# Performance work log

Measured on AMD Instinct MI355X. Metric: run time of the kernel, lower is better.

## Reference

```python
import jax, jax.numpy as jnp
import numpy as np

D_MODEL = 2048
NUM_HEADS = 16
D_K = D_MODEL // NUM_HEADS
LORA_R = 8
LORA_ALPHA = 16
SCALING = LORA_ALPHA / LORA_R  # 2.0
B, S = 2, 2048


def setup_inputs() -> dict:
    key = jax.random.key(0)
    ks = jax.random.split(key, 17)
    s = 1.0 / np.sqrt(D_MODEL)
    d = {"x": jax.random.normal(ks[0], (B, S, D_MODEL), jnp.float32)}
    i = 1
    for name in ("q", "k", "v", "o"):
        d[f"W{name}"] = jax.random.uniform(ks[i], (D_MODEL, D_MODEL), jnp.float32, -s, s); i += 1
        d[f"b{name}"] = jax.random.uniform(ks[i], (D_MODEL,), jnp.float32, -s, s); i += 1
        d[f"A{name}"] = jax.random.uniform(ks[i], (LORA_R, D_MODEL), jnp.float32, -s, s); i += 1
        # lora_B is zero-initialized in the module, but use small random so grads flow meaningfully
        d[f"B{name}"] = jax.random.normal(ks[i], (D_MODEL, LORA_R), jnp.float32) * 0.01; i += 1
    return d


def _lora_linear(x, W, b, A, Bm):
    # F.linear(x, W, b) + (x @ A.T @ B.T) * scaling
    return x @ W.T + b + ((x @ A.T) @ Bm.T) * SCALING


def reference(x, Wq, bq, Aq, Bq, Wk, bk, Ak, Bk, Wv, bv, Av, Bv, Wo, bo, Ao, Bo):
    batch = x.shape[0]
    q = _lora_linear(x, Wq, bq, Aq, Bq)
    k = _lora_linear(x, Wk, bk, Ak, Bk)
    v = _lora_linear(x, Wv, bv, Av, Bv)
    # [B, S, H, Dk] -> [B, H, S, Dk]
    q = q.reshape(batch, -1, NUM_HEADS, D_K).transpose(0, 2, 1, 3)
    k = k.reshape(batch, -1, NUM_HEADS, D_K).transpose(0, 2, 1, 3)
    v = v.reshape(batch, -1, NUM_HEADS, D_K).transpose(0, 2, 1, 3)
    scores = jnp.einsum("bhqd,bhkd->bhqk", q, k) / jnp.sqrt(jnp.float32(D_K))
    attn = jax.nn.softmax(scores, axis=-1)
    context = jnp.einsum("bhqk,bhkd->bhqd", attn, v)
    context = context.transpose(0, 2, 1, 3).reshape(batch, -1, D_MODEL)
    return _lora_linear(context, Wo, bo, Ao, Bo)
```

## Files before the change

### kernel.cpp

```cpp
#include <hip/hip_runtime.h>
#include <stdint.h>

typedef unsigned short u16;
typedef unsigned int   u32;
typedef __bf16  bf16x8 __attribute__((ext_vector_type(8)));
typedef float   f32x4  __attribute__((ext_vector_type(4)));

#define LORA_SCALE 2.0f
#define QSCALE 0.08838834764831845f
#define LOG2E  1.4426950408889634f
#define RESCALE_THR 8.0f

__device__ __forceinline__ u16 f2bf(float f){
  u32 u = __builtin_bit_cast(u32, f);
  u32 r = (u + 0x7fffu + ((u >> 16) & 1u)) >> 16;
  return (u16)r;
}
__device__ __forceinline__ float bf2f(u16 v){
  return __builtin_bit_cast(float, ((u32)v) << 16);
}
__device__ __forceinline__ u32 cvt_pk_bf16(float lo, float hi){
  u32 d;
  asm("v_cvt_pk_bf16_f32 %0, %1, %2" : "=v"(d) : "v"(lo), "v"(hi));
  return d;
}

typedef __attribute__((address_space(3))) u32 lds_u32_t;
typedef __attribute__((address_space(1))) const u32 g_u32_t;

__device__ __forceinline__ void gload16(const void* g, void* l){
  __builtin_amdgcn_global_load_lds((g_u32_t*)(unsigned long long)g,
                                   (lds_u32_t*)(u32)(unsigned long long)l,
                                   16, 0, 0);
}

__global__ __launch_bounds__(256) void cvt_w4(const float* __restrict__ W0,
    const float* __restrict__ W1, const float* __restrict__ W2,
    const float* __restrict__ W3, u16* __restrict__ wqkv, u16* __restrict__ wo){
  int sel = blockIdx.x >> 11;
  int inner = blockIdx.x & 2047;
  const float* src = sel==0 ? W0 : sel==1 ? W1 : sel==2 ? W2 : W3;
  u16* dst = sel<3 ? (wqkv + (size_t)sel*4194304) : wo;
  int i = (inner*256 + threadIdx.x) * 8;
  float4 a = *(const float4*)(src + i);
  float4 b = *(const float4*)(src + i + 4);
  u16 o[8] = {f2bf(a.x),f2bf(a.y),f2bf(a.z),f2bf(a.w),
              f2bf(b.x),f2bf(b.y),f2bf(b.z),f2bf(b.w)};
  *(uint4*)(dst + i) = *(const uint4*)o;
}

__global__ __launch_bounds__(256) void lora_x_fused(const float* __restrict__ x,
    const float* __restrict__ A0, const float* __restrict__ A1, const float* __restrict__ A2,
    float* __restrict__ xout, u16* __restrict__ xbf){
  int w = threadIdx.x >> 6, lane = threadIdx.x & 63;
  int m = blockIdx.x * 4 + w;
  float acc[3][8];
  #pragma unroll
  for (int g=0; g<3; ++g)
    #pragma unroll
    for (int r=0; r<8; ++r) acc[g][r] = 0.f;
  const float* As[3] = {A0, A1, A2};
  #pragma unroll 1
  for (int it=0; it<8; ++it){
    int k = it*256 + lane*4;
    float4 xv = *(const float4*)(x + (size_t)m*2048 + k);
    u16 o[4] = {f2bf(xv.x), f2bf(xv.y), f2bf(xv.z), f2bf(xv.w)};
    *(uint2*)(xbf + (size_t)m*2048 + k) = *(const uint2*)o;
    #pragma unroll
    for (int g=0; g<3; ++g){
      const float* Ag = As[g];
      #pragma unroll
      for (int r=0; r<8; ++r){
        float4 av = *(const float4*)(Ag + r*2048 + k);
        acc[g][r] += xv.x*av.x + xv.y*av.y + xv.z*av.z + xv.w*av.w;
      }
    }
  }
  #pragma unroll
  for (int g=0; g<3; ++g)
    #pragma unroll
    for (int r=0; r<8; ++r){
      float v = acc[g][r];
      #pragma unroll
      for (int off=32; off; off>>=1) v += __shfl_xor(v, off);
      if (lane == 0) xout[g*32768 + m*8 + r] = v;
    }
}

__global__ __launch_bounds__(256) void lora_xa_bf16(const u16* __restrict__ xin,
    const float* __restrict__ A0, float* __restrict__ xout){
  int w = threadIdx.x >> 6, lane = threadIdx.x & 63;
  int m = blockIdx.x * 4 + w;
  float acc[8];
  #pragma unroll
  for (int r=0; r<8; ++r) acc[r] = 0.f;
  #pragma unroll 1
  for (int it=0; it<8; ++it){
    int k = it*256 + lane*4;
    ushort4 u = *(const ushort4*)(xin + (size_t)m*2048 + k);
    float4 xv = {bf2f(u.x), bf2f(u.y), bf2f(u.z), bf2f(u.w)};
    #pragma unroll
    for (int r=0; r<8; ++r){
      float4 av = *(const float4*)(A0 + r*2048 + k);
      acc[r] += xv.x*av.x + xv.y*av.y + xv.z*av.z + xv.w*av.w;
    }
  }
  #pragma unroll
  for (int r=0; r<8; ++r){
    float v = acc[r];
    #pragma unroll
    for (int off=32; off; off>>=1) v += __shfl_xor(v, off);
    if (lane == 0) xout[m*8 + r] = v;
  }
}

__device__ __forceinline__ void gemm_core_v7(
    const u16* __restrict__ Aptr,
    const u16* __restrict__ Wptr,
    u16* lds, int tid, f32x4 acc[8][4]){
  const int Kd = 2048;
  int l = tid & 63, w = tid >> 6;
  int l15 = l & 15, l4 = l >> 4;
  int wm = w >> 1, wn = w & 1;
  char* L = (char*)lds;
  int wb = w * 1024;
  const u16* asrc[4]; const u16* bsrc[2];
  #pragma unroll
  for (int i=0;i<4;i++){ int row=(i*4+w)*16+(l>>2); int sc=((l&3)^((row>>1)&3))<<3;
    asrc[i] = Aptr + (size_t)row*Kd + sc; }
  #pragma unroll
  for (int i=0;i<2;i++){ int row=(i*4+w)*16+(l>>2); int sc=((l&3)^((row>>1)&3))<<3;
    bsrc[i] = Wptr + (size_t)row*Kd + sc; }
  int aoff[8], boff[4];
  #pragma unroll
  for (int mr=0;mr<8;mr++){ int ra=wm*128+mr*16+l15; aoff[mr]=ra*64+((l4^((ra>>1)&3))<<4); }
  #pragma unroll
  for (int nr=0;nr<4;nr++){ int rb=wn*64+nr*16+l15; boff[nr]=16384+rb*64+((l4^((rb>>1)&3))<<4); }

  auto STG = [&](int kt, int sbase){
    char* D = L + sbase;
    gload16(asrc[0]+kt, D +        wb);
    gload16(asrc[1]+kt, D +  4096+ wb);
    gload16(asrc[2]+kt, D +  8192+ wb);
    gload16(asrc[3]+kt, D + 12288+ wb);
    gload16(bsrc[0]+kt, D + 16384+ wb);
    gload16(bsrc[1]+kt, D + 20480+ wb);
  };

  STG(0, 0); STG(32, 24576);
  asm volatile("s_waitcnt vmcnt(6)" ::: "memory");
  __builtin_amdgcn_s_barrier();

  int bb = 0, sb = 49152, kt2 = 64;
  #pragma unroll 1
  for (int t = 0; t < 64; ++t){
    bf16x8 af[4], bf[4];
    #pragma unroll
    for (int mr=0;mr<4;mr++) af[mr] = *(const bf16x8*)(L + bb + aoff[mr]);
    #pragma unroll
    for (int nr=0;nr<4;nr++) bf[nr] = *(const bf16x8*)(L + bb + boff[nr]);
    if (t < 62) STG(kt2, sb);
    __builtin_amdgcn_s_barrier();
    __builtin_amdgcn_s_setprio(1);
    #pragma unroll
    for (int mr=0;mr<4;mr++)
      #pragma unroll
      for (int nr=0;nr<4;nr++)
        acc[mr][nr] = __builtin_amdgcn_mfma_f32_16x16x32_bf16(af[mr], bf[nr], acc[mr][nr], 0,0,0);
    __builtin_amdgcn_s_setprio(0);
    __builtin_amdgcn_s_barrier();
    bf16x8 ag[4];
    #pragma unroll
    for (int mr=0;mr<4;mr++) ag[mr] = *(const bf16x8*)(L + bb + aoff[mr+4]);
    if (t < 62)       asm volatile("s_waitcnt vmcnt(6)" ::: "memory");
    else if (t == 62) asm volatile("s_waitcnt vmcnt(0)" ::: "memory");
    __builtin_amdgcn_s_barrier();
    __builtin_amdgcn_s_setprio(1);
    #pragma unroll
    for (int mr=0;mr<4;mr++)
      #pragma unroll
      for (int nr=0;nr<4;nr++)
        acc[mr+4][nr] = __builtin_amdgcn_mfma_f32_16x16x32_bf16(ag[mr], bf[nr], acc[mr+4][nr], 0,0,0);
    __builtin_amdgcn_s_setprio(0);
    __builtin_amdgcn_s_barrier();
    bb = (bb == 49152) ? 0 : bb + 24576;
    sb = (sb == 49152) ? 0 : sb + 24576;
    kt2 += 32;
  }
}

__global__ __launch_bounds__(256, 2) void gemm_qkv(
    const u16* __restrict__ A, const u16* __restrict__ W,
    const float* __restrict__ bq, const float* __restrict__ bk, const float* __restrict__ bv,
    const float* __restrict__ lBq, const float* __restrict__ lBk, const float* __restrict__ lBv,
    const float* __restrict__ xa, u16* __restrict__ Qb, u16* __restrict__ Kb, u16* __restrict__ Vb){
  __shared__ u16 lds[36864];
  int tid = threadIdx.x;
  int l = tid & 63, w = tid >> 6;
  int l15 = l & 15, l4 = l >> 4;
  int wm = w >> 1, wn = w & 1;
  int bid = blockIdx.x;
  int virt = (bid & 7) * 96 + (bid >> 3);
  int mt = virt & 15, nt = virt >> 4;
  int m0 = mt * 256, n0g = nt * 128;
  int which = nt >> 4;
  int n0 = (nt & 15) * 128;
  const float* bias = which==0 ? bq : which==1 ? bk : bv;
  const float* lB   = which==0 ? lBq : which==1 ? lBk : lBv;
  const float* xs   = xa + which*32768;
  u16* outp         = which==0 ? Qb : which==1 ? Kb : Vb;
  int swz = (which <= 1);
  float oscale = (which == 0) ? QSCALE*LOG2E : 1.0f;

  f32x4 acc[8][4];
  #pragma unroll
  for (int mr=0; mr<8; mr++)
    #pragma unroll
    for (int nr=0; nr<4; nr++) acc[mr][nr] = (f32x4){0.f,0.f,0.f,0.f};

  gemm_core_v7(A + (size_t)m0*2048, W + (size_t)n0g*2048, lds, tid, acc);

  float bvv[4]; float4 lb0[4], lb1[4];
  #pragma unroll
  for (int nr=0; nr<4; nr++){
    int col = n0 + wn*64 + nr*16 + l15;
    bvv[nr] = bias[col];
    lb0[nr] = *(const float4*)(lB + col*8);
    lb1[nr] = *(const float4*)(lB + col*8 + 4);
  }
  #pragma unroll
  for (int mr=0; mr<8; mr++)
    #pragma unroll
    for (int j=0; j<4; j++){
      int r = m0 + wm*128 + mr*16 + l4*4 + j;
      float4 xv0 = *(const float4*)(xs + (size_t)r*8);
      float4 xv1 = *(const float4*)(xs + (size_t)r*8 + 4);
      #pragma unroll
      for (int nr=0; nr<4; nr++){
        int col = n0 + wn*64 + nr*16 + l15;
        float v = acc[mr][nr][j] + bvv[nr] + LORA_SCALE * (
            xv0.x*lb0[nr].x + xv0.y*lb0[nr].y + xv0.z*lb0[nr].z + xv0.w*lb0[nr].w +
            xv1.x*lb1[nr].x + xv1.y*lb1[nr].y + xv1.z*lb1[nr].z + xv1.w*lb1[nr].w);
        v *= oscale;
        int cs = swz ? (col ^ ((r & 7) << 3)) : col;
        outp[(size_t)r*2048 + cs] = f2bf(v);
      }
    }
}

__global__ __launch_bounds__(256, 2) void gemm_o(
    const u16* __restrict__ A, const u16* __restrict__ W,
    const float* __restrict__ bias, const float* __restrict__ lB,
    const float* __restrict__ xa, float* __restrict__ outp){
  __shared__ u16 lds[36864];
  int tid = threadIdx.x;
  int l = tid & 63, w = tid >> 6;
  int l15 = l & 15, l4 = l >> 4;
  int wm = w >> 1, wn = w & 1;
  int bid = blockIdx.x;
  int virt = (bid & 7) * 32 + (bid >> 3);
  int mt = virt & 15, nt = virt >> 4;
  int m0 = mt * 256, n0 = nt * 128;

  f32x4 acc[8][4];
  #pragma unroll
  for (int mr=0; mr<8; mr++)
    #pragma unroll
    for (int nr=0; nr<4; nr++) acc[mr][nr] = (f32x4){0.f,0.f,0.f,0.f};

  gemm_core_v7(A + (size_t)m0*2048, W + (size_t)n0*2048, lds, tid, acc);

  float bv[4]; float4 lb0[4], lb1[4];
  #pragma unroll
  for (int nr=0; nr<4; nr++){
    int col = n0 + wn*64 + nr*16 + l15;
    bv[nr] = bias[col];
    lb0[nr] = *(const float4*)(lB + col*8);
    lb1[nr] = *(const float4*)(lB + col*8 + 4);
  }
  #pragma unroll
  for (int mr=0; mr<8; mr++)
    #pragma unroll
    for (int j=0; j<4; j++){
      int r = m0 + wm*128 + mr*16 + l4*4 + j;
      float4 xv0 = *(const float4*)(xa + (size_t)r*8);
      float4 xv1 = *(const float4*)(xa + (size_t)r*8 + 4);
      #pragma unroll
      for (int nr=0; nr<4; nr++){
        int col = n0 + wn*64 + nr*16 + l15;
        float v = acc[mr][nr][j] + bv[nr] + LORA_SCALE * (
            xv0.x*lb0[nr].x + xv0.y*lb0[nr].y + xv0.z*lb0[nr].z + xv0.w*lb0[nr].w +
            xv1.x*lb1[nr].x + xv1.y*lb1[nr].y + xv1.z*lb1[nr].z + xv1.w*lb1[nr].w);
        outp[(size_t)r*2048 + col] = v;
      }
    }
}

__global__ __launch_bounds__(256) void transpose_v(const u16* __restrict__ V,
                                                   u16* __restrict__ Vt){
  __shared__ u16 tile[64*80];
  int tid = threadIdx.x;
  int f0 = blockIdx.x * 64, m0 = blockIdx.y * 64;
  int i = tid >> 2, j0 = (tid & 3) * 16;
  #pragma unroll
  for (int kk=0; kk<16; kk+=8){
    uint4 u = *(const uint4*)(V + (size_t)(m0 + i)*2048 + f0 + j0 + kk);
    *(uint4*)(tile + i*80 + j0 + kk) = u;
  }
  __syncthreads();
  int j = tid >> 2, i0 = (tid & 3) * 16;
  int b = m0 >> 11, s0 = m0 & 2047;
  int h = f0 >> 7, d = (f0 & 127) + j;
  int c = (d & 7) << 3;
  size_t obase = ((size_t)((b*16 + h)*128 + d)) * 2048 + s0;
  #pragma unroll
  for (int kk=0; kk<16; kk+=8){
    u16 v8[8];
    #pragma unroll
    for (int u2=0; u2<8; ++u2) v8[u2] = tile[(i0+kk+u2)*80 + j];
    *(uint4*)(Vt + obase + ((i0+kk) ^ c)) = *(const uint4*)v8;
  }
}

__global__ __launch_bounds__(256, 2) void attn_kernel(
    const u16* __restrict__ Q, const u16* __restrict__ K,
    const u16* __restrict__ Vt, u16* __restrict__ ctx){
  __shared__ u16 buf[2][16384];
  __shared__ u16 Psh[4*32*64];
  int tid = threadIdx.x, w = tid >> 6, lane = tid & 63;
  int l15 = lane & 15, l4 = lane >> 4;
  int lin = blockIdx.x;
  int virt = (lin & 7) * 64 + (lin >> 3);
  int qt = virt & 15, bh = virt >> 4;
  int b = bh >> 4, h = bh & 15;
  const u16* Qg = Q + (size_t)(b*2048 + qt*128) * 2048 + h*128;
  const u16* Kg = K + (size_t)(b*2048) * 2048 + h*128;
  const u16* Vg = Vt + (size_t)bh * 128 * 2048;

  #pragma unroll
  for (int i=0; i<8; ++i){
    int e = (i*256 + tid) * 8;
    int r = e >> 7, cc = e & 127;
    gload16(Qg + (size_t)r*2048 + cc, (char*)buf[1] + i*4096 + w*1024);
  }
  #pragma unroll
  for (int i=0; i<4; ++i){
    int e = (i*256 + tid) * 8;
    int r = e >> 7, cc = e & 127;
    gload16(Kg + (size_t)r*2048 + cc, (char*)buf[0] + i*4096 + w*1024);
    int dd = e >> 6, c2 = e & 63;
    gload16(Vg + (size_t)dd*2048 + c2, (char*)buf[0] + 16384 + i*4096 + w*1024);
  }
  __syncthreads();

  bf16x8 qf[2][4];
  #pragma unroll
  for (int mi=0; mi<2; mi++){
    int r = w*32 + mi*16 + l15;
    #pragma unroll
    for (int kb=0; kb<4; kb++){
      int cc = (kb*32 + l4*8) ^ ((r & 7) << 3);
      qf[mi][kb] = *(const bf16x8*)(buf[1] + r*128 + cc);
    }
  }
  __syncthreads();

  f32x4 ctxa[2][8];
  #pragma unroll
  for (int mi=0; mi<2; mi++)
    #pragma unroll
    for (int nd=0; nd<8; nd++) ctxa[mi][nd] = (f32x4){0.f,0.f,0.f,0.f};
  float mrun[2] = {-3.0e38f, -3.0e38f};
  float lrun[2] = {0.f, 0.f};

  char* PwB = (char*)(Psh + w * (32*64));
  int psw = (l15 & 7) << 4;

  for (int t = 0; t < 32; ++t){
    int cur = t & 1;
    const u16* Kc = buf[cur];
    const u16* Vc = buf[cur] + 8192;
    if (t + 1 < 32){
      int kvn = (t + 1) * 64;
      char* bn = (char*)buf[cur ^ 1];
      #pragma unroll
      for (int i=0; i<4; ++i){
        int e = (i*256 + tid) * 8;
        int r = e >> 7, cc = e & 127;
        gload16(Kg + (size_t)(kvn + r)*2048 + cc, bn + i*4096 + w*1024);
        int dd = e >> 6, c2 = e & 63;
        gload16(Vg + (size_t)dd*2048 + kvn + c2, bn + 16384 + i*4096 + w*1024);
      }
    }
    f32x4 s[2][4];
    #pragma unroll
    for (int mi=0; mi<2; mi++)
      #pragma unroll
      for (int ni=0; ni<4; ni++) s[mi][ni] = (f32x4){0.f,0.f,0.f,0.f};
    __builtin_amdgcn_s_setprio(1);
    #pragma unroll
    for (int kb=0; kb<4; kb++){
      #pragma unroll
      for (int ni=0; ni<4; ni++){
        int r = ni*16 + l15;
        int cc = (kb*32 + l4*8) ^ ((r & 7) << 3);
        bf16x8 kf = *(const bf16x8*)(Kc + r*128 + cc);
        s[0][ni] = __builtin_amdgcn_mfma_f32_16x16x32_bf16(kf, qf[0][kb], s[0][ni], 0, 0, 0);
        s[1][ni] = __builtin_amdgcn_mfma_f32_16x16x32_bf16(kf, qf[1][kb], s[1][ni], 0, 0, 0);
      }
    }
    __builtin_amdgcn_s_setprio(0);
    float pm[2];
    #pragma unroll
    for (int mi=0; mi<2; mi++){
      float v = s[mi][0][0];
      #pragma unroll
      for (int ni=0; ni<4; ni++)
        #pragma unroll
        for (int j=0; j<4; j++) v = fmaxf(v, s[mi][ni][j]);
      v = fmaxf(v, __shfl_xor(v, 16));
      v = fmaxf(v, __shfl_xor(v, 32));
      pm[mi] = v;
    }
    bool need = (pm[0] > mrun[0] + RESCALE_THR) || (pm[1] > mrun[1] + RESCALE_THR);
    if (__any(need)){
      #pragma unroll
      for (int mi=0; mi<2; mi++){
        float mnew = fmaxf(mrun[mi], pm[mi]);
        float cr = exp2f(mrun[mi] - mnew);
        lrun[mi] *= cr;
        mrun[mi] = mnew;
        #pragma unroll
        for (int nd=0; nd<8; nd++) ctxa[mi][nd] *= cr;
      }
    }
    #pragma unroll
    for (int mi=0; mi<2; mi++){
      float ps = 0.f;
      #pragma unroll
      for (int ni=0; ni<4; ni++){
        float p0 = exp2f(s[mi][ni][0] - mrun[mi]);
        float p1 = exp2f(s[mi][ni][1] - mrun[mi]);
        float p2 = exp2f(s[mi][ni][2] - mrun[mi]);
        float p3 = exp2f(s[mi][ni][3] - mrun[mi]);
        ps += (p0 + p1) + (p2 + p3);
        uint2 pk = {cvt_pk_bf16(p0, p1), cvt_pk_bf16(p2, p3)};
        *(uint2*)(PwB + (mi*16 + l15)*128 + ((ni*32 + l4*8) ^ psw)) = pk;
      }
      ps += __shfl_xor(ps, 16);
      ps += __shfl_xor(ps, 32);
      lrun[mi] += ps;
    }
    bf16x8 pb[2][2];
    #pragma unroll
    for (int mi=0; mi<2; mi++)
      #pragma unroll
      for (int kvb=0; kvb<2; kvb++)
        pb[mi][kvb] = *(const bf16x8*)(PwB + (mi*16 + l15)*128 + ((kvb*64 + l4*16) ^ psw));
    __builtin_amdgcn_s_setprio(1);
    #pragma unroll
    for (int nd=0; nd<8; nd++){
      int dd = nd*16 + l15;
      int sw = (dd & 7) << 3;
      #pragma unroll
      for (int kvb=0; kvb<2; kvb++){
        bf16x8 vf = *(const bf16x8*)(Vc + dd*64 + ((kvb*32 + l4*8) ^ sw));
        ctxa[0][nd] = __builtin_amdgcn_mfma_f32_16x16x32_bf16(vf, pb[0][kvb], ctxa[0][nd], 0, 0, 0);
        ctxa[1][nd] = __builtin_amdgcn_mfma_f32_16x16x32_bf16(vf, pb[1][kvb], ctxa[1][nd], 0, 0, 0);
      }
    }
    __builtin_amdgcn_s_setprio(0);
    __syncthreads();
  }
  char* OwB = (char*)buf[0] + w*8192;
  #pragma unroll
  for (int mi=0; mi<2; mi++){
    float inv = 1.0f / lrun[mi];
    #pragma unroll
    for (int nd=0; nd<8; nd++){
      f32x4 c = ctxa[mi][nd] * inv;
      uint2 pk = {cvt_pk_bf16(c[0], c[1]), cvt_pk_bf16(c[2], c[3])};
      *(uint2*)(OwB + (mi*16 + l15)*256 + ((nd*32 + l4*8) ^ psw)) = pk;
    }
  }
  #pragma unroll
  for (int i=0; i<8; ++i){
    int row = i*4 + l4;
    int colb = l15*16;
    uint4 v = *(const uint4*)(OwB + row*256 + (colb ^ ((row & 7) << 4)));
    int srow = qt*128 + w*32 + row;
    *(uint4*)(ctx + ((size_t)(b*2048 + srow))*2048 + h*128 + colb/2) = v;
  }
}

extern "C" void kernel_launch(void* const* d_in, const int* in_sizes, int n_in,
                              void* d_out, int out_size, void* d_ws, size_t ws_size,
                              hipStream_t stream){
  const float* x  = (const float*)d_in[0];
  const float* Wq = (const float*)d_in[1];  const float* bq = (const float*)d_in[2];
  const float* Aq = (const float*)d_in[3];  const float* Bq = (const float*)d_in[4];
  const float* Wk = (const float*)d_in[5];  const float* bk = (const float*)d_in[6];
  const float* Ak = (const float*)d_in[7];  const float* Bk = (const float*)d_in[8];
  const float* Wv = (const float*)d_in[9];  const float* bv = (const float*)d_in[10];
  const float* Av = (const float*)d_in[11]; const float* Bv = (const float*)d_in[12];
  const float* Wo = (const float*)d_in[13]; const float* bo = (const float*)d_in[14];
  const float* Ao = (const float*)d_in[15]; const float* Bo = (const float*)d_in[16];

  char* ws = (char*)d_ws;
  size_t off = 0;
  u16* xbf  = (u16*)(ws + off); off += (size_t)4096*2048*2;
  u16* wqkv = (u16*)(ws + off); off += (size_t)3*2048*2048*2;
  u16* wob  = (u16*)(ws + off); off += (size_t)2048*2048*2;
  float* xa = (float*)(ws + off); off += (size_t)4*32768*4;
  u16* Qb  = (u16*)(ws + off); off += (size_t)4096*2048*2;
  u16* Kb  = (u16*)(ws + off); off += (size_t)4096*2048*2;
  u16* Vb  = (u16*)(ws + off); off += (size_t)4096*2048*2;
  u16* Vtb = (u16*)(ws + off); off += (size_t)4096*2048*2;
  if (ws_size < off) return;

  cvt_w4<<<8192, 256, 0, stream>>>(Wq, Wk, Wv, Wo, wqkv, wob);
  lora_x_fused<<<1024, 256, 0, stream>>>(x, Aq, Ak, Av, xa, xbf);

  gemm_qkv<<<768, 256, 0, stream>>>(xbf, wqkv, bq, bk, bv, Bq, Bk, Bv, xa, Qb, Kb, Vb);

  transpose_v<<<dim3(32,64), 256, 0, stream>>>(Vb, Vtb);

  attn_kernel<<<512, 256, 0, stream>>>(Qb, Kb, Vtb, Vb);

  lora_xa_bf16<<<1024, 256, 0, stream>>>(Vb, Ao, xa+98304);

  gemm_o<<<256, 256, 0, stream>>>(Vb, wob, bo, Bo, xa+98304, (float*)d_out);
}
```

Before: 339.9 us.

## Fuse V transpose into QKV GEMM epilogue and block LoRA-A rows per wave

```diff
diff --git a/kernel.cpp b/kernel.cpp
--- a/kernel.cpp
+++ b/kernel.cpp
@@ -53,65 +53,85 @@
     const float* __restrict__ A0, const float* __restrict__ A1, const float* __restrict__ A2,
     float* __restrict__ xout, u16* __restrict__ xbf){
   int w = threadIdx.x >> 6, lane = threadIdx.x & 63;
-  int m = blockIdx.x * 4 + w;
-  float acc[3][8];
-  #pragma unroll
-  for (int g=0; g<3; ++g)
-    #pragma unroll
-    for (int r=0; r<8; ++r) acc[g][r] = 0.f;
+  int m0 = blockIdx.x * 16 + w * 4;
+  float acc[4][3][8];
+  #pragma unroll
+  for (int rr=0; rr<4; ++rr)
+    #pragma unroll
+    for (int g=0; g<3; ++g)
+      #pragma unroll
+      for (int r=0; r<8; ++r) acc[rr][g][r] = 0.f;
   const float* As[3] = {A0, A1, A2};
   #pragma unroll 1
   for (int it=0; it<8; ++it){
     int k = it*256 + lane*4;
-    float4 xv = *(const float4*)(x + (size_t)m*2048 + k);
-    u16 o[4] = {f2bf(xv.x), f2bf(xv.y), f2bf(xv.z), f2bf(xv.w)};
-    *(uint2*)(xbf + (size_t)m*2048 + k) = *(const uint2*)o;
+    float4 xv[4];
+    #pragma unroll
+    for (int rr=0; rr<4; ++rr){
+      xv[rr] = *(const float4*)(x + (size_t)(m0+rr)*2048 + k);
+      u16 o[4] = {f2bf(xv[rr].x), f2bf(xv[rr].y), f2bf(xv[rr].z), f2bf(xv[rr].w)};
+      *(uint2*)(xbf + (size_t)(m0+rr)*2048 + k) = *(const uint2*)o;
+    }
     #pragma unroll
     for (int g=0; g<3; ++g){
       const float* Ag = As[g];
       #pragma unroll
       for (int r=0; r<8; ++r){
         float4 av = *(const float4*)(Ag + r*2048 + k);
-        acc[g][r] += xv.x*av.x + xv.y*av.y + xv.z*av.z + xv.w*av.w;
-      }
-    }
-  }
-  #pragma unroll
-  for (int g=0; g<3; ++g)
-    #pragma unroll
-    for (int r=0; r<8; ++r){
-      float v = acc[g][r];
-      #pragma unroll
-      for (int off=32; off; off>>=1) v += __shfl_xor(v, off);
-      if (lane == 0) xout[g*32768 + m*8 + r] = v;
-    }
+        #pragma unroll
+        for (int rr=0; rr<4; ++rr)
+          acc[rr][g][r] += xv[rr].x*av.x + xv[rr].y*av.y + xv[rr].z*av.z + xv[rr].w*av.w;
+      }
+    }
+  }
+  #pragma unroll
+  for (int rr=0; rr<4; ++rr)
+    #pragma unroll
+    for (int g=0; g<3; ++g)
+      #pragma unroll
+      for (int r=0; r<8; ++r){
+        float v = acc[rr][g][r];
+        #pragma unroll
+        for (int off=32; off; off>>=1) v += __shfl_xor(v, off);
+        if (lane == 0) xout[g*32768 + (m0+rr)*8 + r] = v;
+      }
 }
 
 __global__ __launch_bounds__(256) void lora_xa_bf16(const u16* __restrict__ xin,
     const float* __restrict__ A0, float* __restrict__ xout){
   int w = threadIdx.x >> 6, lane = threadIdx.x & 63;
-  int m = blockIdx.x * 4 + w;
-  float acc[8];
-  #pragma unroll
-  for (int r=0; r<8; ++r) acc[r] = 0.f;
+  int m0 = blockIdx.x * 16 + w * 4;
+  float acc[4][8];
+  #pragma unroll
+  for (int rr=0; rr<4; ++rr)
+    #pragma unroll
+    for (int r=0; r<8; ++r) acc[rr][r] = 0.f;
   #pragma unroll 1
   for (int it=0; it<8; ++it){
     int k = it*256 + lane*4;
-    ushort4 u = *(const ushort4*)(xin + (size_t)m*2048 + k);
-    float4 xv = {bf2f(u.x), bf2f(u.y), bf2f(u.z), bf2f(u.w)};
+    float4 xv[4];
+    #pragma unroll
+    for (int rr=0; rr<4; ++rr){
+      ushort4 u = *(const ushort4*)(xin + (size_t)(m0+rr)*2048 + k);
+      xv[rr] = (float4){bf2f(u.x), bf2f(u.y), bf2f(u.z), bf2f(u.w)};
+    }
     #pragma unroll
     for (int r=0; r<8; ++r){
       float4 av = *(const float4*)(A0 + r*2048 + k);
-      acc[r] += xv.x*av.x + xv.y*av.y + xv.z*av.z + xv.w*av.w;
-    }
-  }
-  #pragma unroll
-  for (int r=0; r<8; ++r){
-    float v = acc[r];
-    #pragma unroll
-    for (int off=32; off; off>>=1) v += __shfl_xor(v, off);
-    if (lane == 0) xout[m*8 + r] = v;
-  }
+      #pragma unroll
+      for (int rr=0; rr<4; ++rr)
+        acc[rr][r] += xv[rr].x*av.x + xv[rr].y*av.y + xv[rr].z*av.z + xv[rr].w*av.w;
+    }
+  }
+  #pragma unroll
+  for (int rr=0; rr<4; ++rr)
+    #pragma unroll
+    for (int r=0; r<8; ++r){
+      float v = acc[rr][r];
+      #pragma unroll
+      for (int off=32; off; off>>=1) v += __shfl_xor(v, off);
+      if (lane == 0) xout[(m0+rr)*8 + r] = v;
+    }
 }
 
 __device__ __forceinline__ void gemm_core_v7(
@@ -193,24 +213,22 @@
     const u16* __restrict__ A, const u16* __restrict__ W,
     const float* __restrict__ bq, const float* __restrict__ bk, const float* __restrict__ bv,
     const float* __restrict__ lBq, const float* __restrict__ lBk, const float* __restrict__ lBv,
-    const float* __restrict__ xa, u16* __restrict__ Qb, u16* __restrict__ Kb, u16* __restrict__ Vb){
+    const float* __restrict__ xa, u16* __restrict__ Qb, u16* __restrict__ Kb, u16* __restrict__ Vtb){
   __shared__ u16 lds[36864];
   int tid = threadIdx.x;
   int l = tid & 63, w = tid >> 6;
   int l15 = l & 15, l4 = l >> 4;
   int wm = w >> 1, wn = w & 1;
   int bid = blockIdx.x;
-  int virt = (bid & 7) * 96 + (bid >> 3);
-  int mt = virt & 15, nt = virt >> 4;
+  int xcd = bid & 7, local = bid >> 3;
+  int mt = xcd*2 + (local >= 48);
+  int nt = (local < 48) ? local : local - 48;
   int m0 = mt * 256, n0g = nt * 128;
   int which = nt >> 4;
   int n0 = (nt & 15) * 128;
   const float* bias = which==0 ? bq : which==1 ? bk : bv;
   const float* lB   = which==0 ? lBq : which==1 ? lBk : lBv;
   const float* xs   = xa + which*32768;
-  u16* outp         = which==0 ? Qb : which==1 ? Kb : Vb;
-  int swz = (which <= 1);
-  float oscale = (which == 0) ? QSCALE*LOG2E : 1.0f;
 
   f32x4 acc[8][4];
   #pragma unroll
@@ -228,6 +246,48 @@
     lb0[nr] = *(const float4*)(lB + col*8);
     lb1[nr] = *(const float4*)(lB + col*8 + 4);
   }
+
+  if (which == 2){
+    __syncthreads();
+    char* L = (char*)lds;
+    #pragma unroll
+    for (int mr=0; mr<8; mr++){
+      float vv[4][4];
+      #pragma unroll
+      for (int j=0; j<4; j++){
+        int r = m0 + wm*128 + mr*16 + l4*4 + j;
+        float4 xv0 = *(const float4*)(xs + (size_t)r*8);
+        float4 xv1 = *(const float4*)(xs + (size_t)r*8 + 4);
+        #pragma unroll
+        for (int nr=0; nr<4; nr++)
+          vv[nr][j] = acc[mr][nr][j] + bvv[nr] + LORA_SCALE * (
+              xv0.x*lb0[nr].x + xv0.y*lb0[nr].y + xv0.z*lb0[nr].z + xv0.w*lb0[nr].w +
+              xv1.x*lb1[nr].x + xv1.y*lb1[nr].y + xv1.z*lb1[nr].z + xv1.w*lb1[nr].w);
+      }
+      int s_ = wm*128 + mr*16 + l4*4;
+      #pragma unroll
+      for (int nr=0; nr<4; nr++){
+        int d = wn*64 + nr*16 + l15;
+        uint2 pk = {cvt_pk_bf16(vv[nr][0], vv[nr][1]), cvt_pk_bf16(vv[nr][2], vv[nr][3])};
+        *(uint2*)(L + d*512 + ((s_*2) ^ ((d & 31) << 4))) = pk;
+      }
+    }
+    __syncthreads();
+    int bq_ = m0 >> 11, s0 = m0 & 2047, h = n0 >> 7;
+    u16* vt = Vtb + ((size_t)((bq_*16 + h)*128)) * 2048;
+    #pragma unroll
+    for (int i=0; i<16; ++i){
+      int flat = i*4096 + tid*16;
+      int d = flat >> 9, s2 = flat & 511;
+      uint4 val = *(const uint4*)(L + d*512 + (s2 ^ ((d & 31) << 4)));
+      int sa = s0 + (s2 >> 1);
+      *(uint4*)(vt + (size_t)d*2048 + (sa & ~63) + ((sa & 63) ^ ((d & 7) << 3))) = val;
+    }
+    return;
+  }
+
+  u16* outp = (which == 0) ? Qb : Kb;
+  float oscale = (which == 0) ? QSCALE*LOG2E : 1.0f;
   #pragma unroll
   for (int mr=0; mr<8; mr++)
     #pragma unroll
@@ -242,7 +302,7 @@
             xv0.x*lb0[nr].x + xv0.y*lb0[nr].y + xv0.z*lb0[nr].z + xv0.w*lb0[nr].w +
             xv1.x*lb1[nr].x + xv1.y*lb1[nr].y + xv1.z*lb1[nr].z + xv1.w*lb1[nr].w);
         v *= oscale;
-        int cs = swz ? (col ^ ((r & 7) << 3)) : col;
+        int cs = col ^ ((r & 7) << 3);
         outp[(size_t)r*2048 + cs] = f2bf(v);
       }
     }
@@ -258,8 +318,9 @@
   int l15 = l & 15, l4 = l >> 4;
   int wm = w >> 1, wn = w & 1;
   int bid = blockIdx.x;
-  int virt = (bid & 7) * 32 + (bid >> 3);
-  int mt = virt & 15, nt = virt >> 4;
+  int xcd = bid & 7, local = bid >> 3;
+  int mt = xcd*2 + (local >= 16);
+  int nt = local & 15;
   int m0 = mt * 256, n0 = nt * 128;
 
   f32x4 acc[8][4];
@@ -294,32 +355,6 @@
         outp[(size_t)r*2048 + col] = v;
       }
     }
-}
-
-__global__ __launch_bounds__(256) void transpose_v(const u16* __restrict__ V,
-                                                   u16* __restrict__ Vt){
-  __shared__ u16 tile[64*80];
-  int tid = threadIdx.x;
-  int f0 = blockIdx.x * 64, m0 = blockIdx.y * 64;
-  int i = tid >> 2, j0 = (tid & 3) * 16;
-  #pragma unroll
-  for (int kk=0; kk<16; kk+=8){
-    uint4 u = *(const uint4*)(V + (size_t)(m0 + i)*2048 + f0 + j0 + kk);
-    *(uint4*)(tile + i*80 + j0 + kk) = u;
-  }
-  __syncthreads();
-  int j = tid >> 2, i0 = (tid & 3) * 16;
-  int b = m0 >> 11, s0 = m0 & 2047;
-  int h = f0 >> 7, d = (f0 & 127) + j;
-  int c = (d & 7) << 3;
-  size_t obase = ((size_t)((b*16 + h)*128 + d)) * 2048 + s0;
-  #pragma unroll
-  for (int kk=0; kk<16; kk+=8){
-    u16 v8[8];
-    #pragma unroll
-    for (int u2=0; u2<8; ++u2) v8[u2] = tile[(i0+kk+u2)*80 + j];
-    *(uint4*)(Vt + obase + ((i0+kk) ^ c)) = *(const uint4*)v8;
-  }
 }
 
 __global__ __launch_bounds__(256, 2) void attn_kernel(
@@ -519,15 +554,13 @@
   if (ws_size < off) return;
 
   cvt_w4<<<8192, 256, 0, stream>>>(Wq, Wk, Wv, Wo, wqkv, wob);
-  lora_x_fused<<<1024, 256, 0, stream>>>(x, Aq, Ak, Av, xa, xbf);
-
-  gemm_qkv<<<768, 256, 0, stream>>>(xbf, wqkv, bq, bk, bv, Bq, Bk, Bv, xa, Qb, Kb, Vb);
-
-  transpose_v<<<dim3(32,64), 256, 0, stream>>>(Vb, Vtb);
+  lora_x_fused<<<256, 256, 0, stream>>>(x, Aq, Ak, Av, xa, xbf);
+
+  gemm_qkv<<<768, 256, 0, stream>>>(xbf, wqkv, bq, bk, bv, Bq, Bk, Bv, xa, Qb, Kb, Vtb);
 
   attn_kernel<<<512, 256, 0, stream>>>(Qb, Kb, Vtb, Vb);
 
-  lora_xa_bf16<<<1024, 256, 0, stream>>>(Vb, Ao, xa+98304);
+  lora_xa_bf16<<<256, 256, 0, stream>>>(Vb, Ao, xa+98304);
 
   gemm_o<<<256, 256, 0, stream>>>(Vb, wob, bo, Bo, xa+98304, (float*)d_out);
 }
```

Result: slower. 363.3 us (+6.9%).
